# Optimization experiments

Measured on AMD Instinct MI355X. Metric: run time of the kernel, lower is better.

## Reference

```python
import jax, jax.numpy as jnp
import numpy as np

N_ITERS = 10


def setup_inputs() -> dict:
    key = jax.random.key(0)
    x = jax.random.normal(key, (1, 4096, 8192), dtype=jnp.float32)
    return {"x": x}


def reference(x):
    # x: (1, d, n). Squeeze batch as in fun().
    a = x[0]  # (d, n)
    # sklearn MinMaxScaler(feature_range=(0,1)): per-column (feature) scaling
    data_min = jnp.min(a, axis=0)  # (n,)
    data_max = jnp.max(a, axis=0)  # (n,)
    data_range = data_max - data_min
    safe_range = jnp.where(data_range == 0, 1.0, data_range)  # sklearn's _handle_zeros_in_scale
    arr = (a - data_min) / safe_range  # fit_transform

    def step(arr, i):
        # p = row - mean(row); note abs(p)*sign(p) == p, kept as written for faithfulness
        p = arr - jnp.mean(arr, axis=1, keepdims=True)
        arr = arr * (1.0 - jnp.abs(p) * jnp.sign(p)) + jnp.where(i == 0, 0.001, 0.0)
        return arr, None

    arr, _ = jax.lax.scan(step, arr, jnp.arange(N_ITERS))
    # inverse_transform: X * safe_range + data_min (sklearn uses the zero-safe scale)
    out = arr * safe_range + data_min
    return out.reshape(1, -1, out.shape[-1])
```

## Files before the change

kernel.cpp:

```cpp
#include <hip/hip_runtime.h>

#define DROWS 4096
#define NCOLS 8192
#define RTILE 64
#define NTILES (DROWS / RTILE)


__global__ __launch_bounds__(256) void colminmax_part(const float* __restrict__ x,
                                                      float* __restrict__ pmin,
                                                      float* __restrict__ pmax) {
    int c = blockIdx.x * 1024 + threadIdx.x * 4;
    int r0 = blockIdx.y * RTILE;
    const float* p = x + (size_t)r0 * NCOLS + c;

    float4 mn = *(const float4*)p;
    float4 mx = mn;
#pragma unroll 8
    for (int i = 1; i < RTILE; ++i) {
        float4 v = *(const float4*)(p + (size_t)i * NCOLS);
        mn.x = fminf(mn.x, v.x); mn.y = fminf(mn.y, v.y);
        mn.z = fminf(mn.z, v.z); mn.w = fminf(mn.w, v.w);
        mx.x = fmaxf(mx.x, v.x); mx.y = fmaxf(mx.y, v.y);
        mx.z = fmaxf(mx.z, v.z); mx.w = fmaxf(mx.w, v.w);
    }
    size_t o = (size_t)blockIdx.y * NCOLS + c;
    *(float4*)(pmin + o) = mn;
    *(float4*)(pmax + o) = mx;
}

__global__ __launch_bounds__(256) void finalize_part(const float* __restrict__ pmin,
                                                     const float* __restrict__ pmax,
                                                     float* __restrict__ fmin,
                                                     float* __restrict__ fsr,
                                                     float* __restrict__ finv) {
    int col = blockIdx.x * 256 + threadIdx.x;
    float mn = pmin[col];
    float mx = pmax[col];
#pragma unroll 9
    for (int y = 1; y < NTILES; ++y) {
        mn = fminf(mn, pmin[(size_t)y * NCOLS + col]);
        mx = fmaxf(mx, pmax[(size_t)y * NCOLS + col]);
    }
    float r = mx - mn;
    float sr = (r == 0.0f) ? 1.0f : r;
    fmin[col] = mn;
    fsr[col] = sr;
    finv[col] = 1.0f / sr;
}


__device__ __forceinline__ float block_sum8(float v, float* red, int slot) {
#pragma unroll
    for (int m = 32; m; m >>= 1) v += __shfl_xor(v, m, 64);
    int wid = threadIdx.x >> 6;
    int lane = threadIdx.x & 63;
    if (lane == 0) red[slot * 8 + wid] = v;
    __syncthreads();
    float* r = red + slot * 8;
    return ((r[0] + r[1]) + (r[2] + r[3])) + ((r[4] + r[5]) + (r[6] + r[7]));
}

__global__ __launch_bounds__(512, 8) void rowiter(const float* __restrict__ x,
                                                  const float* __restrict__ fmin,
                                                  const float* __restrict__ fsr,
                                                  const float* __restrict__ finv,
                                                  float* __restrict__ out) {
    int row = blockIdx.x;
    int t = threadIdx.x;
    const float* xr = x + (size_t)row * NCOLS;
    float* outr = out + (size_t)row * NCOLS;

    __shared__ float red[16];

    float4 a[4];
    float psum = 0.0f;
#pragma unroll
    for (int k = 0; k < 4; ++k) {
        int c = k * 2048 + t * 4;
        float4 v = *(const float4*)(xr + c);
        float4 mn = *(const float4*)(fmin + c);
        float4 iv = *(const float4*)(finv + c);
        float4 u;
        u.x = (v.x - mn.x) * iv.x;
        u.y = (v.y - mn.y) * iv.y;
        u.z = (v.z - mn.z) * iv.z;
        u.w = (v.w - mn.w) * iv.w;
        a[k] = u;
        psum += (u.x + u.y) + (u.z + u.w);
    }
    float sum = block_sum8(psum, red, 0);

#pragma unroll
    for (int it = 0; it < 9; ++it) {
        float c1 = 1.0f + sum * (1.0f / 8192.0f);
        float add = (it == 0) ? 0.001f : 0.0f;
        psum = 0.0f;
#pragma unroll
        for (int k = 0; k < 4; ++k) {
            float4 u = a[k];
            u.x = fmaf(u.x, c1 - u.x, add);
            u.y = fmaf(u.y, c1 - u.y, add);
            u.z = fmaf(u.z, c1 - u.z, add);
            u.w = fmaf(u.w, c1 - u.w, add);
            a[k] = u;
            psum += (u.x + u.y) + (u.z + u.w);
        }
        sum = block_sum8(psum, red, (it + 1) & 1);
    }

    {
        float c1 = 1.0f + sum * (1.0f / 8192.0f);
#pragma unroll
        for (int k = 0; k < 4; ++k) {
            int c = k * 2048 + t * 4;
            float4 mn = *(const float4*)(fmin + c);
            float4 sr = *(const float4*)(fsr + c);
            float4 u = a[k];
            u.x = u.x * (c1 - u.x);
            u.y = u.y * (c1 - u.y);
            u.z = u.z * (c1 - u.z);
            u.w = u.w * (c1 - u.w);
            float* o = outr + c;
            __builtin_nontemporal_store(fmaf(u.x, sr.x, mn.x), o + 0);
            __builtin_nontemporal_store(fmaf(u.y, sr.y, mn.y), o + 1);
            __builtin_nontemporal_store(fmaf(u.z, sr.z, mn.z), o + 2);
            __builtin_nontemporal_store(fmaf(u.w, sr.w, mn.w), o + 3);
        }
    }
}

extern "C" void kernel_launch(void* const* d_in, const int* in_sizes, int n_in,
                              void* d_out, int out_size, void* d_ws, size_t ws_size,
                              hipStream_t stream) {
    const float* x = (const float*)d_in[0];
    float* out = (float*)d_out;

    float* pmin = (float*)d_ws;
    float* pmax = pmin + (size_t)NTILES * NCOLS;
    float* fmin = pmax + (size_t)NTILES * NCOLS;
    float* fsr = fmin + NCOLS;
    float* finv = fsr + NCOLS;

    colminmax_part<<<dim3(NCOLS / 1024, NTILES), 256, 0, stream>>>(x, pmin, pmax);
    finalize_part<<<NCOLS / 256, 256, 0, stream>>>(pmin, pmax, fmin, fsr, finv);
    rowiter<<<DROWS, 512, 0, stream>>>(x, fmin, fsr, finv, out);
}
```

Measured before the change: 79.70 us.

## Process several rows per block and prefetch the next row into registers

The row-iteration kernel now launches 1024 blocks of 256 threads instead of 4096 blocks of 512. Each block handles 4 rows strided by 1024, with each thread holding 32 elements. While the current row's 10 reduction iterations run, the next row's input is loaded into registers, so global-load latency overlaps with compute and block synchronisation. In exchange there are fewer resident waves and higher register pressure per thread, and the whole pipeline is already close to memory-bandwidth bound.

```diff
diff --git a/kernel.cpp b/kernel.cpp
--- a/kernel.cpp
+++ b/kernel.cpp
@@ -4,6 +4,8 @@
 #define NCOLS 8192
 #define RTILE 64
 #define NTILES (DROWS / RTILE)
+#define RBLOCKS 1024
+#define ROWS_PER_BLOCK (DROWS / RBLOCKS)
 
 
 __global__ __launch_bounds__(256) void colminmax_part(const float* __restrict__ x,
@@ -49,70 +51,84 @@
 }
 
 
-__device__ __forceinline__ float block_sum8(float v, float* red, int slot) {
+__device__ __forceinline__ float block_sum(float v, float* red, int slot) {
 #pragma unroll
     for (int m = 32; m; m >>= 1) v += __shfl_xor(v, m, 64);
     int wid = threadIdx.x >> 6;
     int lane = threadIdx.x & 63;
-    if (lane == 0) red[slot * 8 + wid] = v;
+    if (lane == 0) red[slot * 4 + wid] = v;
     __syncthreads();
-    float* r = red + slot * 8;
-    return ((r[0] + r[1]) + (r[2] + r[3])) + ((r[4] + r[5]) + (r[6] + r[7]));
+    float* r = red + slot * 4;
+    return (r[0] + r[1]) + (r[2] + r[3]);
 }
 
-__global__ __launch_bounds__(512, 8) void rowiter(const float* __restrict__ x,
+__global__ __launch_bounds__(256, 4) void rowiter(const float* __restrict__ x,
                                                   const float* __restrict__ fmin,
                                                   const float* __restrict__ fsr,
                                                   const float* __restrict__ finv,
                                                   float* __restrict__ out) {
-    int row = blockIdx.x;
     int t = threadIdx.x;
-    const float* xr = x + (size_t)row * NCOLS;
-    float* outr = out + (size_t)row * NCOLS;
+    __shared__ float red[8];
 
-    __shared__ float red[16];
+    float4 v[8];
+    {
+        const float* xr = x + (size_t)blockIdx.x * NCOLS;
+#pragma unroll
+        for (int k = 0; k < 8; ++k)
+            v[k] = *(const float4*)(xr + k * 1024 + t * 4);
+    }
 
-    float4 a[4];
-    float psum = 0.0f;
+    for (int r = 0; r < ROWS_PER_BLOCK; ++r) {
+        size_t row = (size_t)blockIdx.x + (size_t)r * RBLOCKS;
+        float* outr = out + row * NCOLS;
+
+        float4 a[8];
+        float psum = 0.0f;
 #pragma unroll
-    for (int k = 0; k < 4; ++k) {
-        int c = k * 2048 + t * 4;
-        float4 v = *(const float4*)(xr + c);
-        float4 mn = *(const float4*)(fmin + c);
-        float4 iv = *(const float4*)(finv + c);
-        float4 u;
-        u.x = (v.x - mn.x) * iv.x;
-        u.y = (v.y - mn.y) * iv.y;
-        u.z = (v.z - mn.z) * iv.z;
-        u.w = (v.w - mn.w) * iv.w;
-        a[k] = u;
-        psum += (u.x + u.y) + (u.z + u.w);
-    }
-    float sum = block_sum8(psum, red, 0);
-
-#pragma unroll
-    for (int it = 0; it < 9; ++it) {
-        float c1 = 1.0f + sum * (1.0f / 8192.0f);
-        float add = (it == 0) ? 0.001f : 0.0f;
-        psum = 0.0f;
-#pragma unroll
-        for (int k = 0; k < 4; ++k) {
-            float4 u = a[k];
-            u.x = fmaf(u.x, c1 - u.x, add);
-            u.y = fmaf(u.y, c1 - u.y, add);
-            u.z = fmaf(u.z, c1 - u.z, add);
-            u.w = fmaf(u.w, c1 - u.w, add);
+        for (int k = 0; k < 8; ++k) {
+            int c = k * 1024 + t * 4;
+            float4 mn = *(const float4*)(fmin + c);
+            float4 iv = *(const float4*)(finv + c);
+            float4 u;
+            u.x = (v[k].x - mn.x) * iv.x;
+            u.y = (v[k].y - mn.y) * iv.y;
+            u.z = (v[k].z - mn.z) * iv.z;
+            u.w = (v[k].w - mn.w) * iv.w;
             a[k] = u;
             psum += (u.x + u.y) + (u.z + u.w);
         }
-        sum = block_sum8(psum, red, (it + 1) & 1);
-    }
 
-    {
+        if (r < ROWS_PER_BLOCK - 1) {
+            const float* xn = x + (row + RBLOCKS) * NCOLS;
+#pragma unroll
+            for (int k = 0; k < 8; ++k)
+                v[k] = *(const float4*)(xn + k * 1024 + t * 4);
+        }
+
+        float sum = block_sum(psum, red, 0);
+
+#pragma unroll
+        for (int it = 0; it < 9; ++it) {
+            float c1 = 1.0f + sum * (1.0f / 8192.0f);
+            float add = (it == 0) ? 0.001f : 0.0f;
+            psum = 0.0f;
+#pragma unroll
+            for (int k = 0; k < 8; ++k) {
+                float4 u = a[k];
+                u.x = fmaf(u.x, c1 - u.x, add);
+                u.y = fmaf(u.y, c1 - u.y, add);
+                u.z = fmaf(u.z, c1 - u.z, add);
+                u.w = fmaf(u.w, c1 - u.w, add);
+                a[k] = u;
+                psum += (u.x + u.y) + (u.z + u.w);
+            }
+            sum = block_sum(psum, red, (it + 1) & 1);
+        }
+
         float c1 = 1.0f + sum * (1.0f / 8192.0f);
 #pragma unroll
-        for (int k = 0; k < 4; ++k) {
-            int c = k * 2048 + t * 4;
+        for (int k = 0; k < 8; ++k) {
+            int c = k * 1024 + t * 4;
             float4 mn = *(const float4*)(fmin + c);
             float4 sr = *(const float4*)(fsr + c);
             float4 u = a[k];
@@ -143,5 +159,5 @@
 
     colminmax_part<<<dim3(NCOLS / 1024, NTILES), 256, 0, stream>>>(x, pmin, pmax);
     finalize_part<<<NCOLS / 256, 256, 0, stream>>>(pmin, pmax, fmin, fsr, finv);
-    rowiter<<<DROWS, 512, 0, stream>>>(x, fmin, fsr, finv, out);
+    rowiter<<<RBLOCKS, 256, 0, stream>>>(x, fmin, fsr, finv, out);
 }
```

After: 125.3 us. +57.2%, slower.
